# Performance work log

Measured on AMD Instinct MI355X. Metric: run time of the kernel, lower is better.

## Reference

```python
import jax, jax.numpy as jnp
import numpy as np

NUM_HEADS = 16


def setup_inputs() -> dict:
    key = jax.random.key(0)
    k1, k2, k3 = jax.random.split(key, 3)
    B, L, C = 4, 2048, 1024
    x = jax.random.normal(k1, (B, L, C), dtype=jnp.float32)
    W_qkv = jax.random.normal(k2, (C, 3 * C), dtype=jnp.float32) * (C ** -0.5)
    W_proj = jax.random.normal(k3, (C, C), dtype=jnp.float32) * (C ** -0.5)
    b_proj = jnp.zeros((C,), dtype=jnp.float32)
    return {"x": x, "W_qkv": W_qkv, "W_proj": W_proj, "b_proj": b_proj, "coatten": 1024}


def reference(x, W_qkv, W_proj, b_proj, coatten):
    B, L, C = x.shape
    H = NUM_HEADS
    D = C // H
    scale = D ** -0.5
    # qkv projection (no bias), split into per-head q, k, v: [B, H, L, D]
    qkv = (x @ W_qkv).reshape(B, L, 3, H, D).transpose(2, 0, 3, 1, 4)
    q, k, v = qkv[0], qkv[1], qkv[2]
    q1, k1, v1 = q[:, :, :coatten], k[:, :, :coatten], v[:, :, :coatten]
    q2, k2, v2 = q[:, :, coatten:], k[:, :, coatten:], v[:, :, coatten:]
    # cross-attention WITHOUT softmax (dropout_p = 0)
    s1 = jnp.einsum('bhid,bhjd->bhij', q1, k2) * scale  # [B,H,ca,L-ca]
    o1 = jnp.einsum('bhij,bhjd->bhid', s1, v2)          # [B,H,ca,D]
    s2 = jnp.einsum('bhid,bhjd->bhij', q2, k1) * scale  # [B,H,L-ca,ca]
    o2 = jnp.einsum('bhij,bhjd->bhid', s2, v1)          # [B,H,L-ca,D]
    # transpose(1,2) then concat on sequence dim, merge heads
    out = jnp.concatenate([o1.transpose(0, 2, 1, 3), o2.transpose(0, 2, 1, 3)], axis=1)
    out = out.reshape(B, L, C)
    return out @ W_proj + b_proj
```

## Files before the change

### kernel.cpp

```cpp
#include <hip/hip_runtime.h>
#include <stdint.h>

typedef __attribute__((ext_vector_type(8))) short  bf16x8;
typedef __attribute__((ext_vector_type(4))) short  short4v;
typedef __attribute__((ext_vector_type(4))) float  f32x4;
typedef __attribute__((ext_vector_type(4))) float  float4v;

__device__ __forceinline__ unsigned short f2bf(float f) {
  unsigned int u = __builtin_bit_cast(unsigned int, f);
  u += 0x7FFFu + ((u >> 16) & 1u);
  return (unsigned short)(u >> 16);
}
__device__ __forceinline__ float bf2f(unsigned short u) {
  return __builtin_bit_cast(float, (unsigned int)u << 16);
}

__device__ __forceinline__ void async_ld16(const void* g, void* l) {
  __builtin_amdgcn_global_load_lds(
      (const __attribute__((address_space(1))) void*)g,
      (__attribute__((address_space(3))) void*)l,
      16, 0, 0);
}

#define SB()  __builtin_amdgcn_sched_barrier(0)
#define BAR() __builtin_amdgcn_s_barrier()

__global__ __launch_bounds__(256) void prep(
    const float* __restrict__ x, const float* __restrict__ Wqkv,
    const float* __restrict__ Wproj,
    unsigned short* __restrict__ xb, unsigned short* __restrict__ wqkvT,
    unsigned short* __restrict__ wprojT) {
  __shared__ float tile[32][33];
  const int b = blockIdx.x, tid = threadIdx.x;
  if (b < 8192) {
    int i = b * 256 + tid;
    float4v v = *(const float4v*)(x + (size_t)i * 4);
    short4v o;
    o[0] = (short)f2bf(v[0]); o[1] = (short)f2bf(v[1]);
    o[2] = (short)f2bf(v[2]); o[3] = (short)f2bf(v[3]);
    *(short4v*)(xb + (size_t)i * 4) = o;
    return;
  }
  const float* in; unsigned short* out; int R, C, bx, by;
  if (b < 11264) { int t = b - 8192;  in = Wqkv;  out = wqkvT;  R = 1024; C = 3072; bx = t % 96; by = t / 96; }
  else           { int t = b - 11264; in = Wproj; out = wprojT; R = 1024; C = 1024; bx = t & 31; by = t >> 5; }
  const int tx = tid & 31, ty = tid >> 5;
  const int c0 = bx * 32, r0 = by * 32;
  #pragma unroll
  for (int rr = ty; rr < 32; rr += 8)
    tile[rr][tx] = in[(size_t)(r0 + rr) * C + c0 + tx];
  __syncthreads();
  #pragma unroll
  for (int cc = ty; cc < 32; cc += 8)
    out[(size_t)(c0 + cc) * R + r0 + tx] = f2bf(tile[tx][cc]);
}

template<int BF16_OUT>
__global__ __launch_bounds__(512, 2) void gemm8t(
    const unsigned short* __restrict__ A,
    const unsigned short* __restrict__ BT,
    void* __restrict__ Cout, const float* __restrict__ bias,
    int ldc, int K) {
  constexpr int PAN = 16384;
  __shared__ __align__(16) char lds[8 * PAN];
  const int tid = threadIdx.x;
  const int ln = tid & 63, w = tid >> 6;
  const int lr = ln & 15, lq = ln >> 4;
  const int wm = w >> 2, wn = w & 3;

  int wid = blockIdx.y * gridDim.x + blockIdx.x;
  const int nwg = gridDim.x * gridDim.y;
  { const int q = nwg >> 3; wid = (wid & 7) * q + (wid >> 3); }
  const int bm = (wid / gridDim.x) * 256, bn = (wid % gridDim.x) * 256;

  const int srow = tid >> 3;
  const int csw = ((tid & 7) ^ (srow & 7)) * 8;
  const unsigned short* rB0 = BT + (size_t)(bn + srow) * K + csw;
  const unsigned short* rB1 = rB0 + (size_t)128 * K;
  const unsigned short* rA0 = A  + (size_t)(bm + srow) * K + csw;
  const unsigned short* rA1 = rA0 + (size_t)128 * K;
  const size_t rowL1 = (size_t)64 * K;
  char* ldst = lds + tid * 16;

#define STG(slot, src, t) do {                                               \
    async_ld16((src) + (size_t)(t) * 64,         ldst + (slot) * PAN);       \
    async_ld16((src) + (size_t)(t) * 64 + rowL1, ldst + (slot) * PAN + 8192);\
  } while (0)

  const int sw0 = ((0 + lq) ^ (lr & 7)) * 16;
  const int sw1 = ((4 + lq) ^ (lr & 7)) * 16;
  const char* Bbase = lds + ((wn & 1) * 64 + lr) * 128;
  const char* Abase = lds + lr * 128;

  bf16x8 a[4][2], b[4][2];
  f32x4 acc[8][4] = {};

#define READ_B2(Bp, nh)                                                      \
    _Pragma("unroll")                                                        \
    for (int bj = 0; bj < 2; ++bj) {                                         \
      const char* p_ = (Bp) + (nh) * 4096 + bj * 2048;                       \
      b[(nh) * 2 + bj][0] = *(const bf16x8*)(p_ + sw0);                      \
      b[(nh) * 2 + bj][1] = *(const bf16x8*)(p_ + sw1);                      \
    }
#define READ_A(Ap, mh)                                                       \
    _Pragma("unroll")                                                        \
    for (int fi = 0; fi < 4; ++fi) {                                         \
      const char* p_ = (Ap) + fi * 2048;                                     \
      a[fi][0] = *(const bf16x8*)(p_ + sw0);                                 \
      a[fi][1] = *(const bf16x8*)(p_ + sw1);                                 \
    }
#define MFMA16(mh, nh)                                                       \
    __builtin_amdgcn_s_setprio(1);                                           \
    _Pragma("unroll")                                                        \
    for (int fi = 0; fi < 4; ++fi)                                           \
      _Pragma("unroll")                                                      \
      for (int bj = 0; bj < 2; ++bj) {                                       \
        f32x4 t_ = acc[(mh) * 4 + fi][(nh) * 2 + bj];                        \
        t_ = __builtin_amdgcn_mfma_f32_16x16x32_bf16(a[fi][0], b[(nh)*2+bj][0], t_, 0, 0, 0); \
        t_ = __builtin_amdgcn_mfma_f32_16x16x32_bf16(a[fi][1], b[(nh)*2+bj][1], t_, 0, 0, 0); \
        acc[(mh) * 4 + fi][(nh) * 2 + bj] = t_;                              \
      }                                                                      \
    __builtin_amdgcn_s_setprio(0);

  const int NT = K / 64;

  STG(0, rB0, 0); STG(1, rB1, 0); STG(2, rA0, 0); STG(3, rA1, 0);
  STG(4, rB0, 1); STG(5, rB1, 1);
  asm volatile("s_waitcnt vmcnt(4)" ::: "memory");
  SB(); BAR(); SB();

  for (int t = 0; t < NT; ++t) {
    const int par = (t & 1) * 4, opar = ((t + 1) & 1) * 4;
    const char* Ap = Abase + (size_t)(par + 2 + wm) * PAN;
    const char* Bp = Bbase + (size_t)(par + (wn >> 1)) * PAN;
    READ_B2(Bp, 0);
    READ_A(Ap, 0);
    if (t + 1 < NT) STG(opar + 2, rA0, t + 1);
    SB(); BAR();
    asm volatile("s_waitcnt lgkmcnt(0)" ::: "memory");
    SB();
    MFMA16(0, 0);
    READ_B2(Bp, 1);
    if (t + 1 < NT) STG(opar + 3, rA1, t + 1);
    SB(); BAR();
    asm volatile("s_waitcnt lgkmcnt(0)" ::: "memory");
    SB();
    MFMA16(0, 1);
    READ_A(Ap + 8192, 1);
    if (t + 2 < NT) STG(par + 0, rB0, t + 2);
    SB(); BAR();
    asm volatile("s_waitcnt lgkmcnt(0)" ::: "memory");
    SB();
    MFMA16(1, 0);
    if (t + 2 < NT) STG(par + 1, rB1, t + 2);
    SB(); BAR(); SB();
    MFMA16(1, 1);
    if (t < NT - 2)       asm volatile("s_waitcnt vmcnt(4)" ::: "memory");
    else if (t == NT - 2) asm volatile("s_waitcnt vmcnt(0)" ::: "memory");
    SB(); BAR(); SB();
  }
#undef STG
#undef READ_B2
#undef READ_A
#undef MFMA16

  const int c0 = bn + wn * 64 + lr;
  if (BF16_OUT) {
    unsigned short* C = (unsigned short*)Cout;
    #pragma unroll
    for (int mf = 0; mf < 8; ++mf)
      #pragma unroll
      for (int i = 0; i < 4; ++i) {
        size_t r = (size_t)(bm + wm * 128 + (mf >> 2) * 64 + (mf & 3) * 16 + lq * 4 + i);
        #pragma unroll
        for (int nf = 0; nf < 4; ++nf)
          C[r * ldc + c0 + (nf >> 1) * 32 + (nf & 1) * 16] = f2bf(acc[mf][nf][i]);
      }
  } else {
    float* C = (float*)Cout;
    float bv[4];
    #pragma unroll
    for (int nf = 0; nf < 4; ++nf)
      bv[nf] = bias ? bias[c0 + (nf >> 1) * 32 + (nf & 1) * 16] : 0.f;
    #pragma unroll
    for (int mf = 0; mf < 8; ++mf)
      #pragma unroll
      for (int i = 0; i < 4; ++i) {
        size_t r = (size_t)(bm + wm * 128 + (mf >> 2) * 64 + (mf & 3) * 16 + lq * 4 + i);
        #pragma unroll
        for (int nf = 0; nf < 4; ++nf)
          C[r * ldc + c0 + (nf >> 1) * 32 + (nf & 1) * 16] = acc[mf][nf][i] + bv[nf];
      }
  }
}

template<int BF16_OUT>
__global__ __launch_bounds__(512, 1) void gemm128(
    const unsigned short* __restrict__ A, int lda,
    const unsigned short* __restrict__ BT, size_t gstride,
    void* __restrict__ Cout, const float* __restrict__ bias,
    int ldc, int K) {
  constexpr int PAN = 16384;
  __shared__ __align__(16) char lds[6 * PAN];
  const int tid = threadIdx.x;
  const int ln = tid & 63, w = tid >> 6;
  const int lr = ln & 15, lq = ln >> 4;
  const int wm = w >> 2, wn = w & 3;

  int wid = blockIdx.y * gridDim.x + blockIdx.x;
  const int nwg = gridDim.x * gridDim.y;
  { const int q = nwg >> 3; wid = (wid & 7) * q + (wid >> 3); }
  const int bm = (wid / gridDim.x) * 128, bn = (wid % gridDim.x) * 256;

  const int srow = tid >> 3;
  const int csw = ((tid & 7) ^ (srow & 7)) * 8;
  const unsigned short* BTg = BT + (size_t)(bm >> 10) * gstride;
  const unsigned short* rB0 = BTg + (size_t)(bn + srow) * K + csw;
  const unsigned short* rB1 = rB0 + (size_t)128 * K;
  const unsigned short* rA0 = A + (size_t)(bm + srow) * lda + csw;
  const size_t rowB = (size_t)64 * K;
  const size_t rowA = (size_t)64 * lda;
  char* ldst = lds + tid * 16;

#define STGB(slot, src, t) do {                                              \
    async_ld16((src) + (size_t)(t) * 64,        ldst + (slot) * PAN);        \
    async_ld16((src) + (size_t)(t) * 64 + rowB, ldst + (slot) * PAN + 8192); \
  } while (0)
#define STGA(slot, src, t) do {                                              \
    async_ld16((src) + (size_t)(t) * 64,        ldst + (slot) * PAN);        \
    async_ld16((src) + (size_t)(t) * 64 + rowA, ldst + (slot) * PAN + 8192); \
  } while (0)

  const int sw0 = ((0 + lq) ^ (lr & 7)) * 16;
  const int sw1 = ((4 + lq) ^ (lr & 7)) * 16;
  const char* Arow = lds + (wm * 64 + lr) * 128;
  const char* Brow = lds + ((wn & 1) * 64 + lr) * 128;

  bf16x8 a[4], b[4];
  f32x4 acc[4][4] = {};

#define RD(ph_sw, Ap, Bp)                                                    \
    _Pragma("unroll")                                                        \
    for (int nf = 0; nf < 4; ++nf) b[nf] = *(const bf16x8*)((Bp) + nf * 2048 + (ph_sw)); \
    _Pragma("unroll")                                                        \
    for (int fi = 0; fi < 4; ++fi) a[fi] = *(const bf16x8*)((Ap) + fi * 2048 + (ph_sw));
#define MM16()                                                               \
    __builtin_amdgcn_s_setprio(1);                                           \
    _Pragma("unroll")                                                        \
    for (int fi = 0; fi < 4; ++fi)                                           \
      _Pragma("unroll")                                                      \
      for (int nf = 0; nf < 4; ++nf)                                         \
        acc[fi][nf] = __builtin_amdgcn_mfma_f32_16x16x32_bf16(a[fi], b[nf], acc[fi][nf], 0, 0, 0); \
    __builtin_amdgcn_s_setprio(0);

  STGB(0, rB0, 0); STGB(1, rB1, 0); STGA(2, rA0, 0);
  STGB(3, rB0, 1); STGB(4, rB1, 1); STGA(5, rA0, 1);
  asm volatile("s_waitcnt vmcnt(6)" ::: "memory");
  SB(); BAR(); SB();

  const int NT = K / 64;
  for (int t = 0; t < NT; ++t) {
    const int par = (t & 1) * 3;
    const char* Ap = Arow + (par + 2) * PAN;
    const char* Bp = Brow + (par + (wn >> 1)) * PAN;
    RD(sw0, Ap, Bp);
    SB(); BAR();
    asm volatile("s_waitcnt lgkmcnt(0)" ::: "memory");
    SB();
    MM16();
    RD(sw1, Ap, Bp);
    SB(); BAR();
    asm volatile("s_waitcnt lgkmcnt(0)" ::: "memory");
    SB();
    MM16();
    if (t + 2 < NT) {
      STGB(par + 0, rB0, t + 2); STGB(par + 1, rB1, t + 2); STGA(par + 2, rA0, t + 2);
      asm volatile("s_waitcnt vmcnt(6)" ::: "memory");
    } else if (t == NT - 2) {
      asm volatile("s_waitcnt vmcnt(0)" ::: "memory");
    }
    SB(); BAR(); SB();
  }
#undef STGB
#undef STGA
#undef RD
#undef MM16

  const int c0 = bn + wn * 64 + lr;
  if (BF16_OUT) {
    unsigned short* C = (unsigned short*)Cout;
    #pragma unroll
    for (int fi = 0; fi < 4; ++fi)
      #pragma unroll
      for (int i = 0; i < 4; ++i) {
        size_t r = (size_t)(bm + wm * 64 + fi * 16 + lq * 4 + i);
        #pragma unroll
        for (int nf = 0; nf < 4; ++nf)
          C[r * ldc + c0 + (nf >> 1) * 32 + (nf & 1) * 16] = f2bf(acc[fi][nf][i]);
      }
  } else {
    float* C = (float*)Cout;
    float bv[4];
    #pragma unroll
    for (int nf = 0; nf < 4; ++nf)
      bv[nf] = bias ? bias[c0 + (nf >> 1) * 32 + (nf & 1) * 16] : 0.f;
    #pragma unroll
    for (int fi = 0; fi < 4; ++fi)
      #pragma unroll
      for (int i = 0; i < 4; ++i) {
        size_t r = (size_t)(bm + wm * 64 + fi * 16 + lq * 4 + i);
        #pragma unroll
        for (int nf = 0; nf < 4; ++nf)
          C[r * ldc + c0 + (nf >> 1) * 32 + (nf & 1) * 16] = acc[fi][nf][i] + bv[nf];
      }
  }
}

__global__ __launch_bounds__(256) void kv_outer(
    const unsigned short* __restrict__ qkv,
    unsigned short* __restrict__ MT, float scale) {
  const int bid = blockIdx.x;
  const int p = bid & 3, unit = bid >> 2;
  const int b = unit >> 5, h = (unit >> 1) & 15, hf = unit & 1;
  const size_t base = ((size_t)(b * 2048 + hf * 1024)) * 3072 + h * 64;
  const unsigned short* kp = qkv + base + 1024;
  const unsigned short* vp = qkv + base + 2048;
  __shared__ __align__(16) unsigned short kT[64][136];
  __shared__ __align__(16) unsigned short vT[64][136];
  const int tid = threadIdx.x, wv = tid >> 6, ln = tid & 63;
  f32x4 acc[4] = {};
  const int e4 = (tid & 15) * 4;
  const int jr = tid >> 4;
  const int fr = ln & 15, ko = (ln >> 4) * 8;

  for (int j0 = p * 256; j0 < p * 256 + 256; j0 += 128) {
    __syncthreads();
    #pragma unroll
    for (int jj = 0; jj < 128; jj += 16) {
      int j = jj + jr;
      size_t go = (size_t)(j0 + j) * 3072 + e4;
      short4v k4 = *(const short4v*)(kp + go);
      short4v v4 = *(const short4v*)(vp + go);
      #pragma unroll
      for (int t = 0; t < 4; t++) {
        kT[e4 + t][j] = (unsigned short)k4[t];
        vT[e4 + t][j] = (unsigned short)v4[t];
      }
    }
    __syncthreads();
    #pragma unroll
    for (int kk = 0; kk < 128; kk += 32) {
      bf16x8 af = *(const bf16x8*)&kT[wv * 16 + fr][kk + ko];
      #pragma unroll
      for (int n = 0; n < 4; n++) {
        bf16x8 bf2 = *(const bf16x8*)&vT[n * 16 + fr][kk + ko];
        acc[n] = __builtin_amdgcn_mfma_f32_16x16x32_bf16(af, bf2, acc[n], 0, 0, 0);
      }
    }
  }
  unsigned short* outp = MT + (size_t)bid * 4096;
  #pragma unroll
  for (int n = 0; n < 4; n++)
    #pragma unroll
    for (int i = 0; i < 4; i++) {
      int d = n * 16 + fr;
      int e = wv * 16 + (ln >> 4) * 4 + i;
      outp[d * 64 + e] = f2bf(acc[n][i] * scale);
    }
}

__global__ __launch_bounds__(256) void w2k(
    const unsigned short* __restrict__ MTp,
    const unsigned short* __restrict__ wprojT,
    unsigned short* __restrict__ w2t) {
  const int g = blockIdx.x >> 4, h = blockIdx.x & 15;
  const int b = g >> 1, hfq = g & 1;
  const int unit = b * 32 + h * 2 + (1 - hfq);
  const unsigned short* mp = MTp + (size_t)(unit * 4) * 4096;
  __shared__ unsigned short Ms[64][72];
  const int tid = threadIdx.x;
  {
    const int d = tid >> 2, eb = (tid & 3) * 16;
    #pragma unroll
    for (int j = 0; j < 16; ++j) {
      float s = 0.f;
      #pragma unroll
      for (int p = 0; p < 4; ++p)
        s += bf2f(mp[p * 4096 + d * 64 + eb + j]);
      Ms[eb + j][d] = f2bf(s);
    }
  }
  __syncthreads();
  const int w = tid >> 6, ln = tid & 63;
  const int fr = ln & 15, lq = ln >> 4, ko = lq * 8;
  bf16x8 bb[4][2];
  #pragma unroll
  for (int nf = 0; nf < 4; ++nf)
    #pragma unroll
    for (int ks = 0; ks < 2; ++ks)
      bb[nf][ks] = *(const bf16x8*)&Ms[nf * 16 + fr][ks * 32 + ko];
  const unsigned short* ap = wprojT + h * 64;
  unsigned short* op = w2t + (size_t)g * 1048576 + h * 64;
  #pragma unroll 4
  for (int cf = 0; cf < 16; ++cf) {
    const int crow = w * 256 + cf * 16;
    f32x4 acc[4] = {};
    #pragma unroll
    for (int ks = 0; ks < 2; ++ks) {
      bf16x8 a = *(const bf16x8*)(ap + (size_t)(crow + fr) * 1024 + ks * 32 + ko);
      #pragma unroll
      for (int nf = 0; nf < 4; ++nf)
        acc[nf] = __builtin_amdgcn_mfma_f32_16x16x32_bf16(a, bb[nf][ks], acc[nf], 0, 0, 0);
    }
    #pragma unroll
    for (int nf = 0; nf < 4; ++nf)
      #pragma unroll
      for (int i = 0; i < 4; ++i)
        op[(size_t)(crow + lq * 4 + i) * 1024 + nf * 16 + fr] = f2bf(acc[nf][i]);
  }
}

extern "C" void kernel_launch(void* const* d_in, const int* in_sizes, int n_in,
                              void* d_out, int out_size, void* d_ws, size_t ws_size,
                              hipStream_t stream) {
  const float* x     = (const float*)d_in[0];
  const float* Wqkv  = (const float*)d_in[1];
  const float* Wproj = (const float*)d_in[2];
  const float* bproj = (const float*)d_in[3];
  float* out = (float*)d_out;

  char* ws = (char*)d_ws;
  unsigned short* xb     = (unsigned short*)(ws);
  unsigned short* W2T    = (unsigned short*)(ws);
  unsigned short* wqkvT  = (unsigned short*)(ws + 16777216);
  unsigned short* wprojT = (unsigned short*)(ws + 23068672);
  unsigned short* qkv    = (unsigned short*)(ws + 25165824);
  unsigned short* MT     = (unsigned short*)(ws + 75497472);

  prep<<<12288, 256, 0, stream>>>(x, Wqkv, Wproj, xb, wqkvT, wprojT);

  gemm8t<1><<<dim3(8, 32), 512, 0, stream>>>(xb, wqkvT, (void*)qkv, nullptr,
                                             3072, 1024);
  gemm128<1><<<dim3(4, 64), 512, 0, stream>>>(xb, 1024,
                                              wqkvT + (size_t)2048 * 1024, 0,
                                              (void*)(qkv + 2048), nullptr,
                                              3072, 1024);

  kv_outer<<<512, 256, 0, stream>>>(qkv, MT, 0.125f);

  w2k<<<128, 256, 0, stream>>>(MT, wprojT, W2T);

  gemm128<0><<<dim3(4, 64), 512, 0, stream>>>(qkv, 3072,
                                              W2T, (size_t)1048576,
                                              (void*)out, bproj,
                                              1024, 1024);
}
```

Measured before the change: 123.0 us.

## Restructure GEMM main loop to prefetch full A/B tiles two steps ahead

The GEMM main loop changes from staggered per-panel async loads, where A is fetched one step ahead and B two steps ahead, to a uniform scheme. All four panels for tile t+2 are issued together after the MFMAs of tile t, with vmcnt(8) waits. A second A-fragment register set (a2) lets both halves of A be read from LDS before compute, which removes one barrier/lgkmcnt wait per iteration. The cost is more VGPR pressure and burstier global loads that overlap less with compute.

```diff
diff --git a/kernel.cpp b/kernel.cpp
--- a/kernel.cpp
+++ b/kernel.cpp
@@ -92,7 +92,7 @@
   const char* Bbase = lds + ((wn & 1) * 64 + lr) * 128;
   const char* Abase = lds + lr * 128;
 
-  bf16x8 a[4][2], b[4][2];
+  bf16x8 a[4][2], a2[4][2], b[4][2];
   f32x4 acc[8][4] = {};
 
 #define READ_B2(Bp, nh)                                                      \
@@ -102,22 +102,22 @@
       b[(nh) * 2 + bj][0] = *(const bf16x8*)(p_ + sw0);                      \
       b[(nh) * 2 + bj][1] = *(const bf16x8*)(p_ + sw1);                      \
     }
-#define READ_A(Ap, mh)                                                       \
+#define READ_AX(arr, Ap)                                                     \
     _Pragma("unroll")                                                        \
     for (int fi = 0; fi < 4; ++fi) {                                         \
       const char* p_ = (Ap) + fi * 2048;                                     \
-      a[fi][0] = *(const bf16x8*)(p_ + sw0);                                 \
-      a[fi][1] = *(const bf16x8*)(p_ + sw1);                                 \
-    }
-#define MFMA16(mh, nh)                                                       \
+      arr[fi][0] = *(const bf16x8*)(p_ + sw0);                               \
+      arr[fi][1] = *(const bf16x8*)(p_ + sw1);                               \
+    }
+#define MFMA16(arr, mh, nh)                                                  \
     __builtin_amdgcn_s_setprio(1);                                           \
     _Pragma("unroll")                                                        \
     for (int fi = 0; fi < 4; ++fi)                                           \
       _Pragma("unroll")                                                      \
       for (int bj = 0; bj < 2; ++bj) {                                       \
         f32x4 t_ = acc[(mh) * 4 + fi][(nh) * 2 + bj];                        \
-        t_ = __builtin_amdgcn_mfma_f32_16x16x32_bf16(a[fi][0], b[(nh)*2+bj][0], t_, 0, 0, 0); \
-        t_ = __builtin_amdgcn_mfma_f32_16x16x32_bf16(a[fi][1], b[(nh)*2+bj][1], t_, 0, 0, 0); \
+        t_ = __builtin_amdgcn_mfma_f32_16x16x32_bf16(arr[fi][0], b[(nh)*2+bj][0], t_, 0, 0, 0); \
+        t_ = __builtin_amdgcn_mfma_f32_16x16x32_bf16(arr[fi][1], b[(nh)*2+bj][1], t_, 0, 0, 0); \
         acc[(mh) * 4 + fi][(nh) * 2 + bj] = t_;                              \
       }                                                                      \
     __builtin_amdgcn_s_setprio(0);
@@ -125,43 +125,41 @@
   const int NT = K / 64;
 
   STG(0, rB0, 0); STG(1, rB1, 0); STG(2, rA0, 0); STG(3, rA1, 0);
-  STG(4, rB0, 1); STG(5, rB1, 1);
-  asm volatile("s_waitcnt vmcnt(4)" ::: "memory");
+  STG(4, rB0, 1); STG(5, rB1, 1); STG(6, rA0, 1); STG(7, rA1, 1);
+  asm volatile("s_waitcnt vmcnt(8)" ::: "memory");
   SB(); BAR(); SB();
 
   for (int t = 0; t < NT; ++t) {
-    const int par = (t & 1) * 4, opar = ((t + 1) & 1) * 4;
+    const int par = (t & 1) * 4;
     const char* Ap = Abase + (size_t)(par + 2 + wm) * PAN;
     const char* Bp = Bbase + (size_t)(par + (wn >> 1)) * PAN;
     READ_B2(Bp, 0);
-    READ_A(Ap, 0);
-    if (t + 1 < NT) STG(opar + 2, rA0, t + 1);
+    READ_AX(a, Ap);
     SB(); BAR();
     asm volatile("s_waitcnt lgkmcnt(0)" ::: "memory");
     SB();
-    MFMA16(0, 0);
+    MFMA16(a, 0, 0);
     READ_B2(Bp, 1);
-    if (t + 1 < NT) STG(opar + 3, rA1, t + 1);
+    READ_AX(a2, Ap + 8192);
     SB(); BAR();
     asm volatile("s_waitcnt lgkmcnt(0)" ::: "memory");
     SB();
-    MFMA16(0, 1);
-    READ_A(Ap + 8192, 1);
-    if (t + 2 < NT) STG(par + 0, rB0, t + 2);
-    SB(); BAR();
-    asm volatile("s_waitcnt lgkmcnt(0)" ::: "memory");
-    SB();
-    MFMA16(1, 0);
-    if (t + 2 < NT) STG(par + 1, rB1, t + 2);
+    MFMA16(a, 0, 1);
     SB(); BAR(); SB();
-    MFMA16(1, 1);
-    if (t < NT - 2)       asm volatile("s_waitcnt vmcnt(4)" ::: "memory");
-    else if (t == NT - 2) asm volatile("s_waitcnt vmcnt(0)" ::: "memory");
+    MFMA16(a2, 1, 0);
+    MFMA16(a2, 1, 1);
+    if (t + 2 < NT) {
+      STG(par + 0, rB0, t + 2); STG(par + 1, rB1, t + 2);
+      STG(par + 2, rA0, t + 2); STG(par + 3, rA1, t + 2);
+      asm volatile("s_waitcnt vmcnt(8)" ::: "memory");
+    } else if (t == NT - 2) {
+      asm volatile("s_waitcnt vmcnt(0)" ::: "memory");
+    }
     SB(); BAR(); SB();
   }
 #undef STG
 #undef READ_B2
-#undef READ_A
+#undef READ_AX
 #undef MFMA16
 
   const int c0 = bn + wn * 64 + lr;
```

Result: no change. 123.2 us (+0.1%).
